# Optimization experiments

Hardware: AMD Instinct MI355X
Metric: run time of the kernel (lower is better)

The kernel has to match this reference:

```python
import jax, jax.numpy as jnp
import numpy as np

N_NODES = 100000


def spmm(edge_src, edge_dst, edge_val, x):
    """z[dst] += val * x[src] over all edges (COO sparse-dense matmul)."""
    gathered = edge_val[:, None] * x[edge_src]  # [E, d]
    return jax.ops.segment_sum(gathered, edge_dst, num_segments=N_NODES)


def setup_inputs() -> dict:
    key = jax.random.key(0)
    k1, k2, k3, k4, k5, k6 = jax.random.split(key, 6)
    N, E, IN, H, C = N_NODES, 1600000, 256, 128, 40
    features = jax.random.normal(k1, (N, IN), dtype=jnp.float32)
    # xavier_uniform-like init
    b1 = float(np.sqrt(6.0 / (IN + H)))
    b2 = float(np.sqrt(6.0 / (H + C)))
    W1 = jax.random.uniform(k2, (IN, H), dtype=jnp.float32, minval=-b1, maxval=b1)
    W2 = jax.random.uniform(k3, (H, C), dtype=jnp.float32, minval=-b2, maxval=b2)
    edge_src = jax.random.randint(k4, (E,), 0, N, dtype=jnp.int32)
    edge_dst = jnp.sort(jax.random.randint(k5, (E,), 0, N, dtype=jnp.int32))
    # normalized-adjacency-like positive edge weights
    edge_val = jax.random.uniform(k6, (E,), dtype=jnp.float32)
    return {"features": features, "W1": W1, "W2": W2,
            "edge_src": edge_src, "edge_dst": edge_dst, "edge_val": edge_val}


def reference(features, W1, W2, edge_src, edge_dst, edge_val):
    # Decoupled GCN: all dense NN layers first (relu between, none after last) ...
    h = jax.nn.relu(features @ W1)
    h = h @ W2  # [N, num_classes]
    # ... then nlayers (=2) rounds of graph propagation (spmm aggregation)
    h = spmm(edge_src, edge_dst, edge_val, h)
    h = spmm(edge_src, edge_dst, edge_val, h)
    return h
```

## Files before the change

kernel.cpp:

```cpp
#include <hip/hip_runtime.h>
#include <cstddef>
#include <cstdint>

#define IN_DIM 256
#define H_DIM  128
#define C_DIM  40
#define BM     128
#define LDH    136
#define PAD_C  40
#define W2_ROWS 64

typedef short bf16x8 __attribute__((ext_vector_type(8)));
typedef float f32x16 __attribute__((ext_vector_type(16)));
typedef uint  u32x4  __attribute__((ext_vector_type(4)));

__device__ __forceinline__ ushort f2bf(float f) {
  uint u = __builtin_bit_cast(uint, f);
  u += 0x7fffu + ((u >> 16) & 1u);
  return (ushort)(u >> 16);
}
__device__ __forceinline__ float bf2f(uint s) {
  uint u = s << 16;
  return __builtin_bit_cast(float, u);
}
__device__ __forceinline__ uint pack2bf(float a, float b) {
#if __has_builtin(__builtin_amdgcn_cvt_pk_bf16_f32)
  typedef __bf16 bf16v2 __attribute__((ext_vector_type(2)));
  bf16v2 r = __builtin_amdgcn_cvt_pk_bf16_f32(a, b);
  return __builtin_bit_cast(uint, r);
#else
  return (uint)f2bf(a) | ((uint)f2bf(b) << 16);
#endif
}

__global__ void setup_kernel(const int* __restrict__ dst, int E,
                             int* __restrict__ row_ptr, int n1,
                             const float* __restrict__ W1,
                             const float* __restrict__ W2,
                             ushort* __restrict__ w1t,
                             ushort* __restrict__ w2t) {
  int tid = blockIdx.x * blockDim.x + threadIdx.x;
  if (tid < IN_DIM * H_DIM) {
    int k = tid >> 7, n = tid & 127;
    w1t[n * IN_DIM + k] = f2bf(W1[tid]);
  } else if (tid < IN_DIM * H_DIM + W2_ROWS * H_DIM) {
    int i = tid - IN_DIM * H_DIM;
    int n = i >> 7, k = i & 127;
    w2t[i] = (n < C_DIM) ? f2bf(W2[k * C_DIM + n]) : (ushort)0;
  }
  if (tid < n1) {
    int lo = 0, hi = E;
    while (lo < hi) {
      int mid = (lo + hi) >> 1;
      if (dst[mid] < tid) lo = mid + 1; else hi = mid;
    }
    row_ptr[tid] = lo;
  }
}

__global__ __launch_bounds__(256, 3) void fused_dense_kernel(
    const float* __restrict__ feat, const ushort* __restrict__ w1t,
    const ushort* __restrict__ w2t, ushort* __restrict__ z0, int N) {
  __shared__ __align__(16) ushort smem[26112];

  const int t = threadIdx.x;
  const int w = t >> 6, l = t & 63;
  const int nb = blockIdx.x * BM;

  f32x16 acc[4];
#pragma unroll
  for (int tn = 0; tn < 4; ++tn)
#pragma unroll
    for (int r = 0; r < 16; ++r) acc[tn][r] = 0.f;

  int rowA = nb + 32 * w + (l & 31);
  if (rowA >= N) rowA = N - 1;
  const float*  ap = feat + (size_t)rowA * IN_DIM + ((l >> 5) << 3);
  const ushort* bp = w1t + ((l & 31) << 8) + ((l >> 5) << 3);

  float4 Ax[2][2];
  bf16x8 Bx[2][4];

#pragma unroll
  for (int ks = 0; ks < 16; ++ks) {
    const int c = ks & 1;
    if (ks == 0) {
      Ax[0][0] = *(const float4*)(ap + 0);
      Ax[0][1] = *(const float4*)(ap + 4);
#pragma unroll
      for (int tn = 0; tn < 4; ++tn)
        Bx[0][tn] = *(const bf16x8*)(bp + tn * (32 * IN_DIM));
    }
    if (ks < 15) {
      const int n16 = (ks + 1) * 16;
      Ax[c ^ 1][0] = *(const float4*)(ap + n16);
      Ax[c ^ 1][1] = *(const float4*)(ap + n16 + 4);
#pragma unroll
      for (int tn = 0; tn < 4; ++tn)
        Bx[c ^ 1][tn] = *(const bf16x8*)(bp + tn * (32 * IN_DIM) + n16);
    }
    uint4 pk;
    pk.x = pack2bf(Ax[c][0].x, Ax[c][0].y);
    pk.y = pack2bf(Ax[c][0].z, Ax[c][0].w);
    pk.z = pack2bf(Ax[c][1].x, Ax[c][1].y);
    pk.w = pack2bf(Ax[c][1].z, Ax[c][1].w);
    bf16x8 af = __builtin_bit_cast(bf16x8, pk);
#pragma unroll
    for (int tn = 0; tn < 4; ++tn)
      acc[tn] = __builtin_amdgcn_mfma_f32_32x32x16_bf16(af, Bx[c][tn], acc[tn], 0, 0, 0);
  }

#pragma unroll
  for (int tn = 0; tn < 4; ++tn) {
    int col = tn * 32 + (l & 31);
#pragma unroll
    for (int r = 0; r < 16; ++r) {
      int nodeLoc = (r & 3) + 8 * (r >> 2) + 4 * (l >> 5) + 32 * w;
      float v = acc[tn][r];
      smem[nodeLoc * LDH + col] = f2bf(v > 0.f ? v : 0.f);
    }
  }
  {
    int row = t >> 2, c4 = (t & 3) << 5;
    const uint4* src = (const uint4*)(w2t + row * H_DIM + c4);
    uint4* dst = (uint4*)(smem + 128 * LDH + row * LDH + c4);
    dst[0] = src[0];
    dst[1] = src[1];
    dst[2] = src[2];
    dst[3] = src[3];
  }
  __syncthreads();

  f32x16 acc2[2];
#pragma unroll
  for (int tn = 0; tn < 2; ++tn)
#pragma unroll
    for (int r = 0; r < 16; ++r) acc2[tn][r] = 0.f;

  const ushort* Hbase  = smem + (w * 32 + (l & 31)) * LDH + ((l >> 5) << 3);
  const ushort* W2base = smem + 128 * LDH + (l & 31) * LDH + ((l >> 5) << 3);
#pragma unroll
  for (int kb = 0; kb < 8; ++kb) {
    bf16x8 af = *(const bf16x8*)(Hbase + kb * 16);
#pragma unroll
    for (int tn = 0; tn < 2; ++tn) {
      bf16x8 bfr = *(const bf16x8*)(W2base + tn * 32 * LDH + kb * 16);
      acc2[tn] = __builtin_amdgcn_mfma_f32_32x32x16_bf16(af, bfr, acc2[tn], 0, 0, 0);
    }
  }

#pragma unroll
  for (int tn = 0; tn < 2; ++tn) {
    int col = tn * 32 + (l & 31);
    if (col < C_DIM) {
#pragma unroll
      for (int r = 0; r < 16; ++r) {
        int node = nb + 32 * w + (r & 3) + 8 * (r >> 2) + 4 * (l >> 5);
        if (node < N) z0[(size_t)node * PAD_C + col] = f2bf(acc2[tn][r]);
      }
    }
  }
}

__global__ __launch_bounds__(256) void spmm_kernel(
    const int* __restrict__ row_ptr, const int* __restrict__ esrc,
    const float* __restrict__ eval, const ushort* __restrict__ x,
    ushort* __restrict__ zb, float* __restrict__ zf, int N, int out_f32) {
  int node = (blockIdx.x << 2) + (threadIdx.x >> 6);
  if (node >= N) return;
  const int lane = threadIdx.x & 63;
  const int h = lane >> 3;
  const int j = lane & 7;
  const bool act = (j < 5);

  int e   = row_ptr[node];
  int end = row_ptr[node + 1];

  float acc[8];
#pragma unroll
  for (int c = 0; c < 8; ++c) acc[c] = 0.f;

  for (; e + 16 <= end; e += 16) {
    int   s0 = esrc[e + h];
    int   s1 = esrc[e + 8 + h];
    float v0 = eval[e + h];
    float v1 = eval[e + 8 + h];
    if (act) {
      u32x4 a = *(const u32x4*)(x + (size_t)s0 * PAD_C + j * 8);
      u32x4 b = *(const u32x4*)(x + (size_t)s1 * PAD_C + j * 8);
      acc[0] = fmaf(v0, bf2f(a.x & 0xffffu), acc[0]);
      acc[1] = fmaf(v0, bf2f(a.x >> 16),     acc[1]);
      acc[2] = fmaf(v0, bf2f(a.y & 0xffffu), acc[2]);
      acc[3] = fmaf(v0, bf2f(a.y >> 16),     acc[3]);
      acc[4] = fmaf(v0, bf2f(a.z & 0xffffu), acc[4]);
      acc[5] = fmaf(v0, bf2f(a.z >> 16),     acc[5]);
      acc[6] = fmaf(v0, bf2f(a.w & 0xffffu), acc[6]);
      acc[7] = fmaf(v0, bf2f(a.w >> 16),     acc[7]);
      acc[0] = fmaf(v1, bf2f(b.x & 0xffffu), acc[0]);
      acc[1] = fmaf(v1, bf2f(b.x >> 16),     acc[1]);
      acc[2] = fmaf(v1, bf2f(b.y & 0xffffu), acc[2]);
      acc[3] = fmaf(v1, bf2f(b.y >> 16),     acc[3]);
      acc[4] = fmaf(v1, bf2f(b.z & 0xffffu), acc[4]);
      acc[5] = fmaf(v1, bf2f(b.z >> 16),     acc[5]);
      acc[6] = fmaf(v1, bf2f(b.w & 0xffffu), acc[6]);
      acc[7] = fmaf(v1, bf2f(b.w >> 16),     acc[7]);
    }
  }
  for (; e + 8 <= end; e += 8) {
    int   s = esrc[e + h];
    float v = eval[e + h];
    if (act) {
      u32x4 u = *(const u32x4*)(x + (size_t)s * PAD_C + j * 8);
      acc[0] = fmaf(v, bf2f(u.x & 0xffffu), acc[0]);
      acc[1] = fmaf(v, bf2f(u.x >> 16),     acc[1]);
      acc[2] = fmaf(v, bf2f(u.y & 0xffffu), acc[2]);
      acc[3] = fmaf(v, bf2f(u.y >> 16),     acc[3]);
      acc[4] = fmaf(v, bf2f(u.z & 0xffffu), acc[4]);
      acc[5] = fmaf(v, bf2f(u.z >> 16),     acc[5]);
      acc[6] = fmaf(v, bf2f(u.w & 0xffffu), acc[6]);
      acc[7] = fmaf(v, bf2f(u.w >> 16),     acc[7]);
    }
  }
  if (e < end) {
    int ei = e + h;
    int ec = ei < end ? ei : end - 1;
    int   s  = esrc[ec];
    float v0 = eval[ec];
    float v  = ei < end ? v0 : 0.f;
    if (act) {
      u32x4 u = *(const u32x4*)(x + (size_t)s * PAD_C + j * 8);
      acc[0] = fmaf(v, bf2f(u.x & 0xffffu), acc[0]);
      acc[1] = fmaf(v, bf2f(u.x >> 16),     acc[1]);
      acc[2] = fmaf(v, bf2f(u.y & 0xffffu), acc[2]);
      acc[3] = fmaf(v, bf2f(u.y >> 16),     acc[3]);
      acc[4] = fmaf(v, bf2f(u.z & 0xffffu), acc[4]);
      acc[5] = fmaf(v, bf2f(u.z >> 16),     acc[5]);
      acc[6] = fmaf(v, bf2f(u.w & 0xffffu), acc[6]);
      acc[7] = fmaf(v, bf2f(u.w >> 16),     acc[7]);
    }
  }

#pragma unroll
  for (int c = 0; c < 8; ++c) acc[c] += __shfl_xor(acc[c], 8);
#pragma unroll
  for (int c = 0; c < 8; ++c) acc[c] += __shfl_xor(acc[c], 16);
#pragma unroll
  for (int c = 0; c < 8; ++c) acc[c] += __shfl_xor(acc[c], 32);

  if (out_f32) {
    if (lane < 5) {
      float4 o0 = {acc[0], acc[1], acc[2], acc[3]};
      float4 o1 = {acc[4], acc[5], acc[6], acc[7]};
      float* p = zf + (size_t)node * C_DIM + j * 8;
      *(float4*)(p + 0) = o0;
      *(float4*)(p + 4) = o1;
    }
  } else {
    if (lane < 5) {
      uint4 p;
      p.x = (uint)f2bf(acc[0]) | ((uint)f2bf(acc[1]) << 16);
      p.y = (uint)f2bf(acc[2]) | ((uint)f2bf(acc[3]) << 16);
      p.z = (uint)f2bf(acc[4]) | ((uint)f2bf(acc[5]) << 16);
      p.w = (uint)f2bf(acc[6]) | ((uint)f2bf(acc[7]) << 16);
      *(uint4*)(zb + (size_t)node * PAD_C + j * 8) = p;
    }
  }
}

extern "C" void kernel_launch(void* const* d_in, const int* in_sizes, int n_in,
                              void* d_out, int out_size, void* d_ws, size_t ws_size,
                              hipStream_t stream) {
  const float* feat  = (const float*)d_in[0];
  const float* W1    = (const float*)d_in[1];
  const float* W2    = (const float*)d_in[2];
  const int*   esrc  = (const int*)d_in[3];
  const int*   edst  = (const int*)d_in[4];
  const float* evalp = (const float*)d_in[5];
  float* out = (float*)d_out;

  const int N = in_sizes[0] / IN_DIM;
  const int E = in_sizes[3];

  char* ws = (char*)d_ws;
  ushort* z0  = (ushort*)ws;
  ushort* z1  = (ushort*)(ws + (size_t)N * PAD_C * 2);
  ushort* w1t = (ushort*)(ws + (size_t)N * PAD_C * 4);
  ushort* w2t = w1t + IN_DIM * H_DIM;
  int* row_ptr = (int*)((char*)(w2t + W2_ROWS * H_DIM));

  setup_kernel<<<(N + 1 + 255) / 256, 256, 0, stream>>>(
      edst, E, row_ptr, N + 1, W1, W2, w1t, w2t);
  fused_dense_kernel<<<(N + BM - 1) / BM, 256, 0, stream>>>(feat, w1t, w2t, z0, N);
  spmm_kernel<<<(N + 3) / 4, 256, 0, stream>>>(row_ptr, esrc, evalp, z0, z1, nullptr, N, 0);
  spmm_kernel<<<(N + 3) / 4, 256, 0, stream>>>(row_ptr, esrc, evalp, z1, nullptr, out, N, 1);
}
```

Before: 301.9 us.

## Pre-pack features and W1 into bf16 MFMA fragment layout in setup kernel

The setup kernel now converts the whole fp32 feature matrix to bf16 and stores it, together with W1, in the exact per-lane MFMA fragment order. The dense GEMM kernel can then load contiguous 16-byte fragments per lane with no in-loop conversion. This trades one extra full pass over the features (read fp32, write bf16) plus a workspace buffer for cheaper, coalesced loads in the GEMM. Because the features were already read only once before, the total memory traffic grows.

```diff
diff --git a/kernel.cpp b/kernel.cpp
--- a/kernel.cpp
+++ b/kernel.cpp
@@ -9,6 +9,8 @@
 #define LDH    136
 #define PAD_C  40
 #define W2_ROWS 64
+#define STEP   512
+#define RBSLAB 8192
 
 typedef short bf16x8 __attribute__((ext_vector_type(8)));
 typedef float f32x16 __attribute__((ext_vector_type(16)));
@@ -37,35 +39,63 @@
                              int* __restrict__ row_ptr, int n1,
                              const float* __restrict__ W1,
                              const float* __restrict__ W2,
-                             ushort* __restrict__ w1t,
-                             ushort* __restrict__ w2t) {
+                             const float* __restrict__ feat,
+                             ushort* __restrict__ feat_frag,
+                             ushort* __restrict__ b_frag,
+                             ushort* __restrict__ w2t,
+                             int N, int feat_items) {
   int tid = blockIdx.x * blockDim.x + threadIdx.x;
-  if (tid < IN_DIM * H_DIM) {
-    int k = tid >> 7, n = tid & 127;
-    w1t[n * IN_DIM + k] = f2bf(W1[tid]);
-  } else if (tid < IN_DIM * H_DIM + W2_ROWS * H_DIM) {
-    int i = tid - IN_DIM * H_DIM;
-    int n = i >> 7, k = i & 127;
-    w2t[i] = (n < C_DIM) ? f2bf(W2[k * C_DIM + n]) : (ushort)0;
-  }
-  if (tid < n1) {
+  if (tid < feat_items) {
+    int l = tid & 63, ks = (tid >> 6) & 15, rb = tid >> 10;
+    int row = rb * 32 + (l & 31); if (row >= N) row = N - 1;
+    int col = ks * 16 + ((l >> 5) << 3);
+    const float4* p = (const float4*)(feat + (size_t)row * IN_DIM + col);
+    float4 v0 = p[0], v1 = p[1];
+    uint4 pk;
+    pk.x = pack2bf(v0.x, v0.y);
+    pk.y = pack2bf(v0.z, v0.w);
+    pk.z = pack2bf(v1.x, v1.y);
+    pk.w = pack2bf(v1.z, v1.w);
+    *(uint4*)(feat_frag + (size_t)tid * 8) = pk;
+    return;
+  }
+  int u = tid - feat_items;
+  if (u < 4096) {
+    int l = u & 63, ks = (u >> 6) & 15, tn = u >> 10;
+    int n  = 32 * tn + (l & 31);
+    int k0 = ks * 16 + ((l >> 5) << 3);
+    ushort r[8];
+#pragma unroll
+    for (int j = 0; j < 8; ++j) r[j] = f2bf(W1[(k0 + j) * H_DIM + n]);
+    *(uint4*)(b_frag + u * 8) = *(uint4*)r;
+    return;
+  }
+  u -= 4096;
+  if (u < W2_ROWS * H_DIM) {
+    int n = u >> 7, k = u & 127;
+    w2t[u] = (n < C_DIM) ? f2bf(W2[k * C_DIM + n]) : (ushort)0;
+    return;
+  }
+  u -= W2_ROWS * H_DIM;
+  if (u < n1) {
     int lo = 0, hi = E;
     while (lo < hi) {
       int mid = (lo + hi) >> 1;
-      if (dst[mid] < tid) lo = mid + 1; else hi = mid;
-    }
-    row_ptr[tid] = lo;
+      if (dst[mid] < u) lo = mid + 1; else hi = mid;
+    }
+    row_ptr[u] = lo;
   }
 }
 
 __global__ __launch_bounds__(256, 3) void fused_dense_kernel(
-    const float* __restrict__ feat, const ushort* __restrict__ w1t,
+    const ushort* __restrict__ feat_frag, const ushort* __restrict__ b_frag,
     const ushort* __restrict__ w2t, ushort* __restrict__ z0, int N) {
   __shared__ __align__(16) ushort smem[26112];
 
   const int t = threadIdx.x;
   const int w = t >> 6, l = t & 63;
   const int nb = blockIdx.x * BM;
+  const int rb = blockIdx.x * 4 + w;
 
   f32x16 acc[4];
 #pragma unroll
@@ -73,41 +103,28 @@
 #pragma unroll
     for (int r = 0; r < 16; ++r) acc[tn][r] = 0.f;
 
-  int rowA = nb + 32 * w + (l & 31);
-  if (rowA >= N) rowA = N - 1;
-  const float*  ap = feat + (size_t)rowA * IN_DIM + ((l >> 5) << 3);
-  const ushort* bp = w1t + ((l & 31) << 8) + ((l >> 5) << 3);
-
-  float4 Ax[2][2];
+  const ushort* ap = feat_frag + (size_t)rb * RBSLAB + l * 8;
+  const ushort* bp = b_frag + l * 8;
+
+  bf16x8 Ax[2];
   bf16x8 Bx[2][4];
+  Ax[0] = *(const bf16x8*)(ap);
+#pragma unroll
+  for (int tn = 0; tn < 4; ++tn)
+    Bx[0][tn] = *(const bf16x8*)(bp + tn * (16 * STEP));
 
 #pragma unroll
   for (int ks = 0; ks < 16; ++ks) {
     const int c = ks & 1;
-    if (ks == 0) {
-      Ax[0][0] = *(const float4*)(ap + 0);
-      Ax[0][1] = *(const float4*)(ap + 4);
+    if (ks < 15) {
+      Ax[c ^ 1] = *(const bf16x8*)(ap + (ks + 1) * STEP);
 #pragma unroll
       for (int tn = 0; tn < 4; ++tn)
-        Bx[0][tn] = *(const bf16x8*)(bp + tn * (32 * IN_DIM));
-    }
-    if (ks < 15) {
-      const int n16 = (ks + 1) * 16;
-      Ax[c ^ 1][0] = *(const float4*)(ap + n16);
-      Ax[c ^ 1][1] = *(const float4*)(ap + n16 + 4);
-#pragma unroll
-      for (int tn = 0; tn < 4; ++tn)
-        Bx[c ^ 1][tn] = *(const bf16x8*)(bp + tn * (32 * IN_DIM) + n16);
-    }
-    uint4 pk;
-    pk.x = pack2bf(Ax[c][0].x, Ax[c][0].y);
-    pk.y = pack2bf(Ax[c][0].z, Ax[c][0].w);
-    pk.z = pack2bf(Ax[c][1].x, Ax[c][1].y);
-    pk.w = pack2bf(Ax[c][1].z, Ax[c][1].w);
-    bf16x8 af = __builtin_bit_cast(bf16x8, pk);
+        Bx[c ^ 1][tn] = *(const bf16x8*)(bp + tn * (16 * STEP) + (ks + 1) * STEP);
+    }
 #pragma unroll
     for (int tn = 0; tn < 4; ++tn)
-      acc[tn] = __builtin_amdgcn_mfma_f32_32x32x16_bf16(af, Bx[c][tn], acc[tn], 0, 0, 0);
+      acc[tn] = __builtin_amdgcn_mfma_f32_32x32x16_bf16(Ax[c], Bx[c][tn], acc[tn], 0, 0, 0);
   }
 
 #pragma unroll
@@ -281,16 +298,22 @@
   const int N = in_sizes[0] / IN_DIM;
   const int E = in_sizes[3];
 
+  const int nblk  = (N + BM - 1) / BM;
+  const int rbmax = nblk * 4;
+  const int feat_items = rbmax * 1024;
+
   char* ws = (char*)d_ws;
-  ushort* z0  = (ushort*)ws;
-  ushort* z1  = (ushort*)(ws + (size_t)N * PAD_C * 2);
-  ushort* w1t = (ushort*)(ws + (size_t)N * PAD_C * 4);
-  ushort* w2t = w1t + IN_DIM * H_DIM;
-  int* row_ptr = (int*)((char*)(w2t + W2_ROWS * H_DIM));
-
-  setup_kernel<<<(N + 1 + 255) / 256, 256, 0, stream>>>(
-      edst, E, row_ptr, N + 1, W1, W2, w1t, w2t);
-  fused_dense_kernel<<<(N + BM - 1) / BM, 256, 0, stream>>>(feat, w1t, w2t, z0, N);
+  ushort* z0        = (ushort*)ws;
+  ushort* z1        = (ushort*)(ws + (size_t)N * PAD_C * 2);
+  ushort* feat_frag = (ushort*)(ws + (size_t)N * PAD_C * 4);
+  ushort* b_frag    = feat_frag + (size_t)rbmax * RBSLAB;
+  ushort* w2t       = b_frag + 4 * 16 * STEP;
+  int* row_ptr      = (int*)(w2t + W2_ROWS * H_DIM);
+
+  const int setup_items = feat_items + 4096 + W2_ROWS * H_DIM + (N + 1);
+  setup_kernel<<<(setup_items + 255) / 256, 256, 0, stream>>>(
+      edst, E, row_ptr, N + 1, W1, W2, feat, feat_frag, b_frag, w2t, N, feat_items);
+  fused_dense_kernel<<<nblk, 256, 0, stream>>>(feat_frag, b_frag, w2t, z0, N);
   spmm_kernel<<<(N + 3) / 4, 256, 0, stream>>>(row_ptr, esrc, evalp, z0, z1, nullptr, N, 0);
   spmm_kernel<<<(N + 3) / 4, 256, 0, stream>>>(row_ptr, esrc, evalp, z1, nullptr, out, N, 1);
 }
```

After: 290.5 us. 1.04x faster.
